# Kernel optimization log

Hardware: AMD Instinct MI355X
Metric: run time of the kernel (lower is better)

The kernel has to match this reference:

```python
import jax, jax.numpy as jnp
import numpy as np

B, N, L, D, H = 32, 512, 1024, 512, 8
C = D // H  # 64 channels per head
SCALE = C ** -0.5


def setup_inputs() -> dict:
    key = jax.random.key(0)
    ks = jax.random.split(key, 10)
    inp = {
        "x_q": jax.random.normal(ks[0], (B, N, D), dtype=jnp.float32),
        "x_kv": jax.random.normal(ks[1], (B, L, D), dtype=jnp.float32),
        "pad_mask": jax.random.randint(ks[2], (B, L), 0, 2).astype(bool),
        # projection weights stored (in, out); no bias except o_proj
        "Wq": jax.random.normal(ks[3], (D, D), dtype=jnp.float32) * (D ** -0.5),
        "Wk": jax.random.normal(ks[4], (D, D), dtype=jnp.float32) * (D ** -0.5),
        "Wv": jax.random.normal(ks[5], (D, D), dtype=jnp.float32) * (D ** -0.5),
        "Wo": jax.random.normal(ks[6], (D, D), dtype=jnp.float32) * (D ** -0.5),
        "bo": jnp.zeros((D,), dtype=jnp.float32),
        # relative position bias, shape (1, feat_w*feat_h, num_qk_channels)
        "rpb": jax.random.normal(ks[7], (1, L, D), dtype=jnp.float32) * 0.02,
    }
    return inp


def reference(x_q, x_kv, pad_mask, Wq, Wk, Wv, Wo, bo, rpb):
    # linear projections
    q = jnp.einsum("bnd,de->bne", x_q, Wq)
    k = jnp.einsum("bld,de->ble", x_kv, Wk) + rpb  # rel-pos bias added to K
    v = jnp.einsum("bld,de->ble", x_kv, Wv)
    # split heads: (B, S, H*C) -> (B, H, S, C)
    split = lambda t: t.reshape(t.shape[0], t.shape[1], H, C).transpose(0, 2, 1, 3)
    q, k, v = split(q), split(k), split(v)
    attn = jnp.einsum("bhic,bhjc->bhij", q, k) * SCALE  # (B,H,N,L)
    neg = -jnp.finfo(attn.dtype).max
    attn = jnp.where(pad_mask[:, None, None, :], neg, attn)
    attn = jax.nn.softmax(attn, axis=-1)
    o = jnp.einsum("bhij,bhjc->bhic", attn, v)
    o = o.transpose(0, 2, 1, 3).reshape(B, N, H * C)  # merge heads
    return jnp.einsum("bnd,de->bne", o, Wo) + bo
```

## Files before the change

kernel.cpp:

```cpp
#include <hip/hip_runtime.h>
#include <hip/hip_bf16.h>

typedef __hip_bfloat16 bf16;
typedef __attribute__((ext_vector_type(8))) short short8;
typedef __attribute__((ext_vector_type(4))) float f32x4;
typedef __attribute__((ext_vector_type(16))) float f32x16;

#define B_SZ 32
#define N_SZ 512
#define L_SZ 1024
#define D_SZ 512
#define H_SZ 8

__device__ __forceinline__ void gload16(void* lds, const void* g) {
    typedef const __attribute__((address_space(1))) unsigned int* gp_t;
    typedef __attribute__((address_space(3))) unsigned int* lp_t;
    __builtin_amdgcn_global_load_lds((gp_t)g, (lp_t)lds, 16, 0, 0);
}

__device__ __forceinline__ unsigned int cvtpk(float lo, float hi) {
    unsigned int r;
    asm("v_cvt_pk_bf16_f32 %0, %1, %2" : "=v"(r) : "v"(lo), "v"(hi));
    return r;
}

__device__ __forceinline__ float fexp2(float x) {
    float r;
    asm("v_exp_f32 %0, %1" : "=v"(r) : "v"(x));
    return r;
}

struct alignas(8) B4 { bf16 a, b, c, d; };

__global__ void cvt_all(const float* __restrict__ xq, const float* __restrict__ xkv,
                        bf16* __restrict__ dq, bf16* __restrict__ dkv) {
    int i = blockIdx.x * 256 + threadIdx.x;
    const float* s;
    bf16* d;
    if (i < 2097152) {
        s = xq; d = dq;
    } else {
        i -= 2097152; s = xkv; d = dkv;
    }
    float4 v = ((const float4*)s)[i];
    B4 o;
    o.a = __float2bfloat16(v.x);
    o.b = __float2bfloat16(v.y);
    o.c = __float2bfloat16(v.z);
    o.d = __float2bfloat16(v.w);
    *(B4*)(d + (size_t)i * 4) = o;
}

__global__ void tpose4(const float* __restrict__ s0, const float* __restrict__ s1,
                       const float* __restrict__ s2, const float* __restrict__ s3,
                       bf16* __restrict__ d0, bf16* __restrict__ d1,
                       bf16* __restrict__ d2, bf16* __restrict__ d3) {
    __shared__ float t[32][33];
    const float* s = blockIdx.z == 0 ? s0 : blockIdx.z == 1 ? s1 : blockIdx.z == 2 ? s2 : s3;
    bf16* d = blockIdx.z == 0 ? d0 : blockIdx.z == 1 ? d1 : blockIdx.z == 2 ? d2 : d3;
    int tx = threadIdx.x, ty = threadIdx.y;
    int r0 = blockIdx.y * 32, c0 = blockIdx.x * 32;
#pragma unroll
    for (int i = 0; i < 32; i += 8)
        t[ty + i][tx] = s[(size_t)(r0 + ty + i) * 512 + c0 + tx];
    __syncthreads();
#pragma unroll
    for (int i = 0; i < 32; i += 8)
        d[(size_t)(c0 + ty + i) * 512 + r0 + tx] = __float2bfloat16(t[tx][ty + i]);
}

__global__ __launch_bounds__(256) void gemm_qkv(
    const bf16* __restrict__ xq, const bf16* __restrict__ xkv,
    const bf16* __restrict__ WqT, const bf16* __restrict__ WkT,
    const bf16* __restrict__ WvT, const float* __restrict__ rpb,
    bf16* __restrict__ qh, bf16* __restrict__ kh, bf16* __restrict__ vTh) {
    __shared__ bf16 lA[128 * 64];
    __shared__ bf16 lB[128 * 64];
    const int tid = threadIdx.x;
    const int wave = tid >> 6, lane = tid & 63;
    const int wr = wave >> 1, wc = wave & 1;
    const int g16 = lane >> 4, r16 = lane & 15;

    int bid = blockIdx.x;
    int mode;
    long rowBase;
    int colBase;
    const bf16 *A, *Bt;
    if (bid < 512) {
        mode = 0; A = xq; Bt = WqT;
        rowBase = (long)(bid >> 2) * 128; colBase = (bid & 3) * 128;
    } else if (bid < 1536) {
        mode = 1; int t = bid - 512; A = xkv; Bt = WkT;
        rowBase = (long)(t >> 2) * 128; colBase = (t & 3) * 128;
    } else {
        mode = 2; int t = bid - 1536; A = WvT; Bt = xkv;
        rowBase = (long)(t & 3) * 128; colBase = (t >> 2) * 128;
    }

    f32x4 acc[4][4];
#pragma unroll
    for (int m = 0; m < 4; ++m)
#pragma unroll
        for (int n = 0; n < 4; ++n) acc[m][n] = {0.f, 0.f, 0.f, 0.f};

    for (int k0 = 0; k0 < 512; k0 += 64) {
        __syncthreads();
#pragma unroll
        for (int rnd = 0; rnd < 4; ++rnd) {
            int chunk = rnd * 256 + tid;
            int row = chunk >> 3, j = chunk & 7, gj = j ^ (row & 7);
            gload16((char*)lA + chunk * 16, A + (rowBase + row) * 512 + k0 + gj * 8);
            gload16((char*)lB + chunk * 16, Bt + (long)(colBase + row) * 512 + k0 + gj * 8);
        }
        __syncthreads();
#pragma unroll
        for (int kk = 0; kk < 2; ++kk) {
            short8 a[4], b[4];
#pragma unroll
            for (int m = 0; m < 4; ++m) {
                int row = wr * 64 + m * 16 + r16;
                a[m] = *(const short8*)((const char*)lA + row * 128 +
                                        (((kk * 4 + g16) ^ (row & 7)) * 16));
            }
#pragma unroll
            for (int n = 0; n < 4; ++n) {
                int row = wc * 64 + n * 16 + r16;
                b[n] = *(const short8*)((const char*)lB + row * 128 +
                                        (((kk * 4 + g16) ^ (row & 7)) * 16));
            }
#pragma unroll
            for (int m = 0; m < 4; ++m)
#pragma unroll
                for (int n = 0; n < 4; ++n)
                    acc[m][n] =
                        __builtin_amdgcn_mfma_f32_16x16x32_bf16(a[m], b[n], acc[m][n], 0, 0, 0);
        }
    }

#pragma unroll
    for (int m = 0; m < 4; ++m) {
#pragma unroll
        for (int r = 0; r < 4; ++r) {
            long gm = rowBase + wr * 64 + m * 16 + g16 * 4 + r;
            if (mode == 2) {
                int e = (int)gm;
                int hh = e >> 6, c = e & 63;
#pragma unroll
                for (int n = 0; n < 4; ++n) {
                    int gl = colBase + wc * 64 + n * 16 + r16;
                    int bb = gl >> 10, s = gl & 1023;
                    vTh[(((long)bb * H_SZ + hh) * 64 + c) * (long)L_SZ + s] =
                        __float2bfloat16(acc[m][n][r]);
                }
            } else if (mode == 1) {
                int bb = (int)(gm >> 10), s = (int)gm & 1023;
#pragma unroll
                for (int n = 0; n < 4; ++n) {
                    int e = colBase + wc * 64 + n * 16 + r16;
                    float v = acc[m][n][r] + rpb[(long)s * 512 + e];
                    int hh = e >> 6, c = e & 63;
                    kh[(((long)bb * H_SZ + hh) * (long)L_SZ + s) * 64 + c] = __float2bfloat16(v);
                }
            } else {
                int bb = (int)(gm >> 9), s = (int)gm & 511;
#pragma unroll
                for (int n = 0; n < 4; ++n) {
                    int e = colBase + wc * 64 + n * 16 + r16;
                    int hh = e >> 6, c = e & 63;
                    qh[(((long)bb * H_SZ + hh) * (long)N_SZ + s) * 64 + c] =
                        __float2bfloat16(acc[m][n][r]);
                }
            }
        }
    }
}

__global__ __launch_bounds__(256) void gemm_o(const bf16* __restrict__ A,
                                              const bf16* __restrict__ Bt,
                                              float* __restrict__ outp,
                                              const float* __restrict__ bias) {
    __shared__ bf16 lA[128 * 64];
    __shared__ bf16 lB[128 * 64];
    const int tid = threadIdx.x;
    const int wave = tid >> 6, lane = tid & 63;
    const int wr = wave >> 1, wc = wave & 1;
    const int g16 = lane >> 4, r16 = lane & 15;
    const long rowBase = (long)blockIdx.x * 128;
    const int colBase = blockIdx.y * 128;

    f32x4 acc[4][4];
#pragma unroll
    for (int m = 0; m < 4; ++m)
#pragma unroll
        for (int n = 0; n < 4; ++n) acc[m][n] = {0.f, 0.f, 0.f, 0.f};

    for (int k0 = 0; k0 < 512; k0 += 64) {
        __syncthreads();
#pragma unroll
        for (int rnd = 0; rnd < 4; ++rnd) {
            int chunk = rnd * 256 + tid;
            int row = chunk >> 3, j = chunk & 7, gj = j ^ (row & 7);
            gload16((char*)lA + chunk * 16, A + (rowBase + row) * 512 + k0 + gj * 8);
            gload16((char*)lB + chunk * 16, Bt + (long)(colBase + row) * 512 + k0 + gj * 8);
        }
        __syncthreads();
#pragma unroll
        for (int kk = 0; kk < 2; ++kk) {
            short8 a[4], b[4];
#pragma unroll
            for (int m = 0; m < 4; ++m) {
                int row = wr * 64 + m * 16 + r16;
                a[m] = *(const short8*)((const char*)lA + row * 128 +
                                        (((kk * 4 + g16) ^ (row & 7)) * 16));
            }
#pragma unroll
            for (int n = 0; n < 4; ++n) {
                int row = wc * 64 + n * 16 + r16;
                b[n] = *(const short8*)((const char*)lB + row * 128 +
                                        (((kk * 4 + g16) ^ (row & 7)) * 16));
            }
#pragma unroll
            for (int m = 0; m < 4; ++m)
#pragma unroll
                for (int n = 0; n < 4; ++n)
                    acc[m][n] =
                        __builtin_amdgcn_mfma_f32_16x16x32_bf16(a[m], b[n], acc[m][n], 0, 0, 0);
        }
    }

#pragma unroll
    for (int m = 0; m < 4; ++m) {
#pragma unroll
        for (int r = 0; r < 4; ++r) {
            long gm = rowBase + wr * 64 + m * 16 + g16 * 4 + r;
#pragma unroll
            for (int n = 0; n < 4; ++n) {
                int e = colBase + wc * 64 + n * 16 + r16;
                outp[gm * 512 + e] = acc[m][n][r] + bias[e];
            }
        }
    }
}

__global__ __launch_bounds__(512, 4) void attn256(const bf16* __restrict__ q,
                                                  const bf16* __restrict__ k,
                                                  const bf16* __restrict__ vT,
                                                  const int* __restrict__ mask,
                                                  bf16* __restrict__ o) {
    __shared__ bf16 lK[2][64 * 64];
    __shared__ bf16 lV[2][64 * 64];
    __shared__ float lMf[1024];

    const int tid = threadIdx.x;
    const int wv = tid >> 6, lane = tid & 63;
    const int q32 = lane & 31, hi = lane >> 5;

    const int wg = blockIdx.x;
    const int xcd = wg & 7, slot = wg >> 3;
    const int bh = xcd * 32 + (slot >> 1), qc = slot & 1;
    const int b = bh >> 3, h = bh & 7;

    const bf16* kbase = k + (long)bh * L_SZ * 64;
    const bf16* vbase = vT + (long)bh * 64 * L_SZ;

    const int* mrow = mask + b * L_SZ;
    lMf[tid] = mrow[tid] ? -1e38f : 0.f;
    lMf[tid + 512] = mrow[tid + 512] ? -1e38f : 0.f;

    const int r_ = tid >> 3, j_ = tid & 7;
    const int gj_ = (j_ ^ (r_ & 7)) * 8;
    const bf16* gK = kbase + r_ * 64 + gj_;
    const bf16* gV = vbase + (long)r_ * L_SZ + gj_;
    char* dK0 = (char*)(&lK[0][0]) + tid * 16;
    char* dK1 = (char*)(&lK[1][0]) + tid * 16;
    char* dV0 = (char*)(&lV[0][0]) + tid * 16;
    char* dV1 = (char*)(&lV[1][0]) + tid * 16;
    gload16(dK0, gK);
    gload16(dV0, gV);

    const bf16* qp = q + ((long)bh * N_SZ + qc * 256 + wv * 32 + q32) * 64 + hi * 8;
    short8 qf[4];
#pragma unroll
    for (int t = 0; t < 4; ++t) qf[t] = *(const short8*)(qp + t * 16);

    float mrun = 0.f, lrun = 0.f;
    f32x16 oa0, oa1;
#pragma unroll
    for (int i = 0; i < 16; ++i) { oa0[i] = 0.f; oa1[i] = 0.f; }

    __syncthreads();

    const float CL = 0.18033688011112042f;

    for (int kb = 0; kb < 16; ++kb) {
        const char* curK = (const char*)(&lK[kb & 1][0]);
        const char* curV = (const char*)(&lV[kb & 1][0]);
        if (kb < 15) {
            gload16((kb & 1) ? dK0 : dK1, gK + (kb + 1) * 4096);
            gload16((kb & 1) ? dV0 : dV1, gV + (kb + 1) * 64);
        }

        f32x16 sA, sB;
#pragma unroll
        for (int i = 0; i < 16; ++i) { sA[i] = 0.f; sB[i] = 0.f; }
#pragma unroll
        for (int t = 0; t < 4; ++t) {
            int sl = ((t * 2 + hi) ^ (q32 & 7)) * 16;
            short8 kfA = *(const short8*)(curK + q32 * 128 + sl);
            short8 kfB = *(const short8*)(curK + (32 + q32) * 128 + sl);
            sA = __builtin_amdgcn_mfma_f32_32x32x16_bf16(kfA, qf[t], sA, 0, 0, 0);
            sB = __builtin_amdgcn_mfma_f32_32x32x16_bf16(kfB, qf[t], sB, 0, 0, 0);
        }

        const float* mf = lMf + kb * 64 + hi * 4;
        float4 ma0 = *(const float4*)(mf);
        float4 ma1 = *(const float4*)(mf + 8);
        float4 ma2 = *(const float4*)(mf + 16);
        float4 ma3 = *(const float4*)(mf + 24);
        float4 mb0 = *(const float4*)(mf + 32);
        float4 mb1 = *(const float4*)(mf + 40);
        float4 mb2 = *(const float4*)(mf + 48);
        float4 mb3 = *(const float4*)(mf + 56);
        float mba[16] = {ma0.x, ma0.y, ma0.z, ma0.w, ma1.x, ma1.y, ma1.z, ma1.w,
                         ma2.x, ma2.y, ma2.z, ma2.w, ma3.x, ma3.y, ma3.z, ma3.w};
        float mbb[16] = {mb0.x, mb0.y, mb0.z, mb0.w, mb1.x, mb1.y, mb1.z, mb1.w,
                         mb2.x, mb2.y, mb2.z, mb2.w, mb3.x, mb3.y, mb3.z, mb3.w};

        float t32[32];
#pragma unroll
        for (int i = 0; i < 16; ++i) {
            t32[i] = fmaf(sA[i], CL, mba[i]);
            t32[16 + i] = fmaf(sB[i], CL, mbb[i]);
        }

        float m16[16];
#pragma unroll
        for (int i = 0; i < 16; ++i) m16[i] = fmaxf(t32[i], t32[16 + i]);
        float m8[8];
#pragma unroll
        for (int i = 0; i < 8; ++i) m8[i] = fmaxf(m16[i], m16[i + 8]);
        float tm = fmaxf(fmaxf(fmaxf(m8[0], m8[4]), fmaxf(m8[1], m8[5])),
                         fmaxf(fmaxf(m8[2], m8[6]), fmaxf(m8[3], m8[7])));
        tm = fmaxf(tm, __shfl_xor(tm, 32));

        if (__any(tm > mrun + 8.f)) {
            float mnew = fmaxf(mrun, tm);
            float al = fexp2(mrun - mnew);
            mrun = mnew;
            lrun *= al;
#pragma unroll
            for (int i = 0; i < 16; ++i) { oa0[i] *= al; oa1[i] *= al; }
        }

#pragma unroll
        for (int i = 0; i < 32; ++i) t32[i] = fexp2(t32[i] - mrun);
        float s16[16];
#pragma unroll
        for (int i = 0; i < 16; ++i) s16[i] = t32[i] + t32[16 + i];
        float s8[8];
#pragma unroll
        for (int i = 0; i < 8; ++i) s8[i] = s16[i] + s16[i + 8];
        float ps = ((s8[0] + s8[4]) + (s8[1] + s8[5])) + ((s8[2] + s8[6]) + (s8[3] + s8[7]));
        ps += __shfl_xor(ps, 32);
        lrun += ps;

        union U { unsigned int u[4]; short8 s8v; };
        U fr[4];
#pragma unroll
        for (int fkt = 0; fkt < 4; ++fkt) {
            const float* tp = t32 + fkt * 8;
            unsigned int y0 = cvtpk(tp[0], tp[1]);
            unsigned int y1 = cvtpk(tp[2], tp[3]);
            unsigned int y2 = cvtpk(tp[4], tp[5]);
            unsigned int y3 = cvtpk(tp[6], tp[7]);
            asm("v_permlane32_swap_b32 %0, %1" : "+v"(y0), "+v"(y2));
            asm("v_permlane32_swap_b32 %0, %1" : "+v"(y1), "+v"(y3));
            fr[fkt].u[0] = y0; fr[fkt].u[1] = y1; fr[fkt].u[2] = y2; fr[fkt].u[3] = y3;
        }

#pragma unroll
        for (int kt = 0; kt < 4; ++kt) {
            int sw = ((kt * 2 + hi) ^ (q32 & 7)) * 16;
            short8 v0 = *(const short8*)(curV + q32 * 128 + sw);
            short8 v1 = *(const short8*)(curV + (32 + q32) * 128 + sw);
            oa0 = __builtin_amdgcn_mfma_f32_32x32x16_bf16(v0, fr[kt].s8v, oa0, 0, 0, 0);
            oa1 = __builtin_amdgcn_mfma_f32_32x32x16_bf16(v1, fr[kt].s8v, oa1, 0, 0, 0);
        }

        __syncthreads();
    }

    float inv = 1.f / lrun;
    bf16* op = o + ((long)b * N_SZ + qc * 256 + wv * 32 + q32) * 512 + h * 64;
#pragma unroll
    for (int ct = 0; ct < 2; ++ct) {
#pragma unroll
        for (int rq = 0; rq < 4; ++rq) {
            int c0 = ct * 32 + rq * 8 + hi * 4;
            float v0 = (ct ? oa1[rq * 4 + 0] : oa0[rq * 4 + 0]) * inv;
            float v1 = (ct ? oa1[rq * 4 + 1] : oa0[rq * 4 + 1]) * inv;
            float v2 = (ct ? oa1[rq * 4 + 2] : oa0[rq * 4 + 2]) * inv;
            float v3 = (ct ? oa1[rq * 4 + 3] : oa0[rq * 4 + 3]) * inv;
            uint2 st;
            st.x = cvtpk(v0, v1);
            st.y = cvtpk(v2, v3);
            *(uint2*)(op + c0) = st;
        }
    }
}

extern "C" void kernel_launch(void* const* d_in, const int* in_sizes, int n_in,
                              void* d_out, int out_size, void* d_ws, size_t ws_size,
                              hipStream_t stream) {
    const float* x_q  = (const float*)d_in[0];
    const float* x_kv = (const float*)d_in[1];
    const int*   mask = (const int*)d_in[2];
    const float* Wq   = (const float*)d_in[3];
    const float* Wk   = (const float*)d_in[4];
    const float* Wv   = (const float*)d_in[5];
    const float* Wo   = (const float*)d_in[6];
    const float* bo   = (const float*)d_in[7];
    const float* rpb  = (const float*)d_in[8];
    float* out = (float*)d_out;

    char* w = (char*)d_ws;
    bf16* xq_bf  = (bf16*)(w + 0);
    bf16* xkv_bf = (bf16*)(w + 16777216);
    bf16* WqT    = (bf16*)(w + 50331648);
    bf16* WkT    = WqT + 262144;
    bf16* WvT    = WkT + 262144;
    bf16* WoT    = WvT + 262144;
    bf16* qh     = (bf16*)(w + 52428800);
    bf16* kh     = (bf16*)(w + 69206016);
    bf16* vTh    = (bf16*)(w + 102760448);
    bf16* o_bf   = xq_bf;

    cvt_all<<<24576, 256, 0, stream>>>(x_q, x_kv, xq_bf, xkv_bf);
    tpose4<<<dim3(16, 16, 4), dim3(32, 8), 0, stream>>>(Wq, Wk, Wv, Wo, WqT, WkT, WvT, WoT);

    gemm_qkv<<<2560, 256, 0, stream>>>(xq_bf, xkv_bf, WqT, WkT, WvT, rpb, qh, kh, vTh);

    attn256<<<512, 512, 0, stream>>>(qh, kh, vTh, mask, o_bf);

    gemm_o<<<dim3(128, 4), 256, 0, stream>>>(o_bf, WoT, out, bo);
}
```

Before: 184.7 us.

## Double-buffer LDS tiles in projection GEMMs and remap blocks across XCDs

Both projection GEMM kernels now keep two LDS buffers, so the global-to-LDS loads for the next K tile are issued while MFMAs run on the current tile. This replaces the two barriers per iteration with one. Block indices are also permuted so that consecutive tiles sharing inputs land on the same XCD, which should improve L2 reuse. The cost is doubled LDS per block (64KB), which may reduce how many blocks fit on a CU.

```diff
diff --git a/kernel.cpp b/kernel.cpp
--- a/kernel.cpp
+++ b/kernel.cpp
@@ -74,14 +74,15 @@
     const bf16* __restrict__ WqT, const bf16* __restrict__ WkT,
     const bf16* __restrict__ WvT, const float* __restrict__ rpb,
     bf16* __restrict__ qh, bf16* __restrict__ kh, bf16* __restrict__ vTh) {
-    __shared__ bf16 lA[128 * 64];
-    __shared__ bf16 lB[128 * 64];
+    __shared__ char sm[2][32768];
     const int tid = threadIdx.x;
     const int wave = tid >> 6, lane = tid & 63;
     const int wr = wave >> 1, wc = wave & 1;
     const int g16 = lane >> 4, r16 = lane & 15;
 
-    int bid = blockIdx.x;
+    const int orig = blockIdx.x;
+    const int bid = (orig & 7) * 320 + (orig >> 3);
+
     int mode;
     long rowBase;
     int colBase;
@@ -97,36 +98,48 @@
         rowBase = (long)(t & 3) * 128; colBase = (t >> 2) * 128;
     }
 
+    const int row_ = tid >> 3;
+    const int gj_ = ((tid & 7) ^ (row_ & 7)) * 8;
+    const bf16* aSrc = A + (rowBase + row_) * 512 + gj_;
+    const bf16* bSrc = Bt + ((long)colBase + row_) * 512 + gj_;
+
     f32x4 acc[4][4];
 #pragma unroll
     for (int m = 0; m < 4; ++m)
 #pragma unroll
         for (int n = 0; n < 4; ++n) acc[m][n] = {0.f, 0.f, 0.f, 0.f};
 
-    for (int k0 = 0; k0 < 512; k0 += 64) {
-        __syncthreads();
-#pragma unroll
-        for (int rnd = 0; rnd < 4; ++rnd) {
-            int chunk = rnd * 256 + tid;
-            int row = chunk >> 3, j = chunk & 7, gj = j ^ (row & 7);
-            gload16((char*)lA + chunk * 16, A + (rowBase + row) * 512 + k0 + gj * 8);
-            gload16((char*)lB + chunk * 16, Bt + (long)(colBase + row) * 512 + k0 + gj * 8);
-        }
-        __syncthreads();
+#pragma unroll
+    for (int rnd = 0; rnd < 4; ++rnd) {
+        gload16(&sm[0][rnd * 4096 + tid * 16], aSrc + rnd * 16384);
+        gload16(&sm[0][16384 + rnd * 4096 + tid * 16], bSrc + rnd * 16384);
+    }
+    __syncthreads();
+
+    for (int t = 0; t < 8; ++t) {
+        const int cur = t & 1;
+        if (t < 7) {
+            const int nk = (t + 1) * 64;
+#pragma unroll
+            for (int rnd = 0; rnd < 4; ++rnd) {
+                gload16(&sm[cur ^ 1][rnd * 4096 + tid * 16], aSrc + rnd * 16384 + nk);
+                gload16(&sm[cur ^ 1][16384 + rnd * 4096 + tid * 16], bSrc + rnd * 16384 + nk);
+            }
+        }
+        const char* lA = &sm[cur][0];
+        const char* lB = &sm[cur][16384];
 #pragma unroll
         for (int kk = 0; kk < 2; ++kk) {
             short8 a[4], b[4];
 #pragma unroll
             for (int m = 0; m < 4; ++m) {
                 int row = wr * 64 + m * 16 + r16;
-                a[m] = *(const short8*)((const char*)lA + row * 128 +
-                                        (((kk * 4 + g16) ^ (row & 7)) * 16));
+                a[m] = *(const short8*)(lA + row * 128 + (((kk * 4 + g16) ^ (row & 7)) * 16));
             }
 #pragma unroll
             for (int n = 0; n < 4; ++n) {
                 int row = wc * 64 + n * 16 + r16;
-                b[n] = *(const short8*)((const char*)lB + row * 128 +
-                                        (((kk * 4 + g16) ^ (row & 7)) * 16));
+                b[n] = *(const short8*)(lB + row * 128 + (((kk * 4 + g16) ^ (row & 7)) * 16));
             }
 #pragma unroll
             for (int m = 0; m < 4; ++m)
@@ -135,6 +148,7 @@
                     acc[m][n] =
                         __builtin_amdgcn_mfma_f32_16x16x32_bf16(a[m], b[n], acc[m][n], 0, 0, 0);
         }
+        __syncthreads();
     }
 
 #pragma unroll
@@ -179,14 +193,21 @@
                                               const bf16* __restrict__ Bt,
                                               float* __restrict__ outp,
                                               const float* __restrict__ bias) {
-    __shared__ bf16 lA[128 * 64];
-    __shared__ bf16 lB[128 * 64];
+    __shared__ char sm[2][32768];
     const int tid = threadIdx.x;
     const int wave = tid >> 6, lane = tid & 63;
     const int wr = wave >> 1, wc = wave & 1;
     const int g16 = lane >> 4, r16 = lane & 15;
-    const long rowBase = (long)blockIdx.x * 128;
-    const int colBase = blockIdx.y * 128;
+
+    const int orig = blockIdx.x;
+    const int bid = (orig & 7) * 64 + (orig >> 3);
+    const long rowBase = (long)(bid >> 2) * 128;
+    const int colBase = (bid & 3) * 128;
+
+    const int row_ = tid >> 3;
+    const int gj_ = ((tid & 7) ^ (row_ & 7)) * 8;
+    const bf16* aSrc = A + (rowBase + row_) * 512 + gj_;
+    const bf16* bSrc = Bt + ((long)colBase + row_) * 512 + gj_;
 
     f32x4 acc[4][4];
 #pragma unroll
@@ -194,30 +215,37 @@
 #pragma unroll
         for (int n = 0; n < 4; ++n) acc[m][n] = {0.f, 0.f, 0.f, 0.f};
 
-    for (int k0 = 0; k0 < 512; k0 += 64) {
-        __syncthreads();
-#pragma unroll
-        for (int rnd = 0; rnd < 4; ++rnd) {
-            int chunk = rnd * 256 + tid;
-            int row = chunk >> 3, j = chunk & 7, gj = j ^ (row & 7);
-            gload16((char*)lA + chunk * 16, A + (rowBase + row) * 512 + k0 + gj * 8);
-            gload16((char*)lB + chunk * 16, Bt + (long)(colBase + row) * 512 + k0 + gj * 8);
-        }
-        __syncthreads();
+#pragma unroll
+    for (int rnd = 0; rnd < 4; ++rnd) {
+        gload16(&sm[0][rnd * 4096 + tid * 16], aSrc + rnd * 16384);
+        gload16(&sm[0][16384 + rnd * 4096 + tid * 16], bSrc + rnd * 16384);
+    }
+    __syncthreads();
+
+    for (int t = 0; t < 8; ++t) {
+        const int cur = t & 1;
+        if (t < 7) {
+            const int nk = (t + 1) * 64;
+#pragma unroll
+            for (int rnd = 0; rnd < 4; ++rnd) {
+                gload16(&sm[cur ^ 1][rnd * 4096 + tid * 16], aSrc + rnd * 16384 + nk);
+                gload16(&sm[cur ^ 1][16384 + rnd * 4096 + tid * 16], bSrc + rnd * 16384 + nk);
+            }
+        }
+        const char* lA = &sm[cur][0];
+        const char* lB = &sm[cur][16384];
 #pragma unroll
         for (int kk = 0; kk < 2; ++kk) {
             short8 a[4], b[4];
 #pragma unroll
             for (int m = 0; m < 4; ++m) {
                 int row = wr * 64 + m * 16 + r16;
-                a[m] = *(const short8*)((const char*)lA + row * 128 +
-                                        (((kk * 4 + g16) ^ (row & 7)) * 16));
+                a[m] = *(const short8*)(lA + row * 128 + (((kk * 4 + g16) ^ (row & 7)) * 16));
             }
 #pragma unroll
             for (int n = 0; n < 4; ++n) {
                 int row = wc * 64 + n * 16 + r16;
-                b[n] = *(const short8*)((const char*)lB + row * 128 +
-                                        (((kk * 4 + g16) ^ (row & 7)) * 16));
+                b[n] = *(const short8*)(lB + row * 128 + (((kk * 4 + g16) ^ (row & 7)) * 16));
             }
 #pragma unroll
             for (int m = 0; m < 4; ++m)
@@ -226,6 +254,7 @@
                     acc[m][n] =
                         __builtin_amdgcn_mfma_f32_16x16x32_bf16(a[m], b[n], acc[m][n], 0, 0, 0);
         }
+        __syncthreads();
     }
 
 #pragma unroll
@@ -442,5 +471,5 @@
 
     attn256<<<512, 512, 0, stream>>>(qh, kh, vTh, mask, o_bf);
 
-    gemm_o<<<dim3(128, 4), 256, 0, stream>>>(o_bf, WoT, out, bo);
-}
+    gemm_o<<<512, 256, 0, stream>>>(o_bf, WoT, out, bo);
+}
```

Result: faster. 177.1 us (-4.1%).
